# Kernel tuning notes

Measured on AMD Instinct MI355X. Metric: run time of the kernel, lower is better.

Reference implementation:

```python
import jax, jax.numpy as jnp
import numpy as np

D_MODEL = 1024
N_HEADS = 16
D_K = D_MODEL // N_HEADS
B, S = 8, 1024
EPS = 1e-8


def setup_inputs() -> dict:
    key = jax.random.key(0)
    ks = jax.random.split(key, 6)
    scale = 1.0 / np.sqrt(D_MODEL)
    return {
        "Q_in": jax.random.normal(ks[0], (B, S, D_MODEL), jnp.float32),
        "mask": jax.random.randint(ks[1], (B, 1, S, S), 0, 2, jnp.int32),
        "Wq": jax.random.normal(ks[2], (D_MODEL, D_MODEL), jnp.float32) * scale,
        "bq": jnp.zeros((D_MODEL,), jnp.float32),
        "Wk": jax.random.normal(ks[3], (D_MODEL, D_MODEL), jnp.float32) * scale,
        "bk": jnp.zeros((D_MODEL,), jnp.float32),
        "Wv": jax.random.normal(ks[4], (D_MODEL, D_MODEL), jnp.float32) * scale,
        "bv": jnp.zeros((D_MODEL,), jnp.float32),
        "Wo": jax.random.normal(ks[5], (D_MODEL, D_MODEL), jnp.float32) * scale,
        "bo": jnp.zeros((D_MODEL,), jnp.float32),
    }


def reference(Q_in, mask, Wq, bq, Wk, bk, Wv, bv, Wo, bo):
    # QKV projections: [B,S,D] -> [B,H,S,d_k]
    def split_heads(x):
        return x.reshape(B, S, N_HEADS, D_K).transpose(0, 2, 1, 3)

    Q = split_heads(Q_in @ Wq + bq)
    K = split_heads(Q_in @ Wk + bk)
    V = split_heads(Q_in @ Wv + bv)

    # scaled scores [B,H,S,S], standard softmax
    scores = jnp.einsum("bhqd,bhkd->bhqk", Q, K) / jnp.sqrt(
        jnp.asarray(D_K, jnp.float32))
    scores = jax.nn.softmax(scores, axis=-1)
    # non-standard: multiplicative mask AFTER softmax, then row renorm
    scores = scores * mask.astype(scores.dtype)
    attn = scores / (jnp.sum(scores, axis=-1, keepdims=True) + EPS)

    context = jnp.einsum("bhqk,bhkd->bhqd", attn, V)
    context = context.transpose(0, 2, 1, 3).reshape(B, S, D_MODEL)
    return context @ Wo + bo
```

## Files before the change

### kernel.cpp

```cpp
#include <hip/hip_runtime.h>
#include <hip/hip_bf16.h>
#include <stdint.h>

typedef __attribute__((ext_vector_type(4))) float f32x4;
typedef __attribute__((ext_vector_type(8))) __bf16 bf16x8;
typedef unsigned short u16;
typedef unsigned int u32;
typedef unsigned long long u64;

#define NH 16
#define DKK 64
#define QSCALE 0.18033688011112042f

__device__ __forceinline__ u16 f2bf(float f) {
    u32 u = __builtin_bit_cast(u32, f);
    u32 r = (u + 0x7fffu + ((u >> 16) & 1u)) >> 16;
    return (u16)r;
}

__device__ __forceinline__ u16 cvt_bf(float f) {
    __hip_bfloat16 h = __float2bfloat16(f);
    return *reinterpret_cast<u16*>(&h);
}

__device__ __forceinline__ float exp2_fast(float x) {
    return __builtin_amdgcn_exp2f(x);
}

__device__ __forceinline__ void gload16(const void* g, void* l) {
    __builtin_amdgcn_global_load_lds((const __attribute__((address_space(1))) void*)g,
                                     (__attribute__((address_space(3))) void*)l, 16, 0, 0);
}

__global__ __launch_bounds__(256) void k_prep(const float* __restrict__ x,
                                              u16* __restrict__ xb,
                                              const float* __restrict__ wq,
                                              const float* __restrict__ wk,
                                              const float* __restrict__ wv,
                                              const float* __restrict__ wo,
                                              u16* __restrict__ wt,
                                              const int* __restrict__ mask,
                                              u64* __restrict__ mb) {
    int bx = blockIdx.x;
    if (bx < 4096) {
        int i = bx * 256 + threadIdx.x;
        const float4* p = (const float4*)x + (size_t)i * 2;
        float4 a = p[0], b = p[1];
        union { u16 h[8]; uint4 q; } o;
        o.h[0] = f2bf(a.x); o.h[1] = f2bf(a.y); o.h[2] = f2bf(a.z); o.h[3] = f2bf(a.w);
        o.h[4] = f2bf(b.x); o.h[5] = f2bf(b.y); o.h[6] = f2bf(b.z); o.h[7] = f2bf(b.w);
        ((uint4*)xb)[i] = o.q;
    } else if (bx < 8192) {
        int idx = bx - 4096;
        int z = idx >> 10;
        const float* w = (z == 0) ? wq : (z == 1) ? wk : (z == 2) ? wv : wo;
        __shared__ float t[32][33];
        int tx = threadIdx.x & 31, ty = threadIdx.x >> 5;
        int n0 = (idx & 31) * 32, k0 = ((idx >> 5) & 31) * 32;
        for (int rr = 0; rr < 4; ++rr)
            t[ty + rr * 8][tx] = w[(size_t)(k0 + ty + rr * 8) * 1024 + n0 + tx];
        __syncthreads();
        for (int rr = 0; rr < 4; ++rr) {
            int n = n0 + ty + rr * 8;
            wt[((size_t)z * 1024 + n) * 1024 + k0 + tx] = f2bf(t[tx][ty + rr * 8]);
        }
    } else {
        int wid = ((bx - 8192) * 256 + threadIdx.x) >> 6;
        int lane = threadIdx.x & 63;
        for (int c = wid; c < 8 * 1024 * 16; c += 8192) {
            int m = mask[(size_t)c * 64 + lane];
            u64 bits = __ballot(m != 0);
            if (lane == 0)
                mb[(c & 0xFFFFC000u) | ((c & 15) << 10) | ((c >> 4) & 1023)] = bits;
        }
    }
}

template <int MODE>
__global__ __launch_bounds__(256) void k_gemm(const u16* __restrict__ A,
                                              const u16* __restrict__ Bt,
                                              const float* __restrict__ b0,
                                              const float* __restrict__ b1,
                                              const float* __restrict__ b2,
                                              u16* __restrict__ q_out,
                                              u16* __restrict__ k_out,
                                              u16* __restrict__ v_out,
                                              float* __restrict__ out) {
    __shared__ u16 As[128 * 32];
    __shared__ u16 Bs[128 * 32];
    int tid = threadIdx.x;
    int wv = tid >> 6, lane = tid & 63;
    int r = lane & 15, g = lane >> 4;
    int wr = wv >> 1, wc = wv & 1;
    int m0 = blockIdx.x * 128, n0 = blockIdx.y * 128;
    f32x4 acc[4][4] = {};
    for (int kt = 0; kt < 1024; kt += 32) {
        __syncthreads();
        for (int i = 0; i < 2; ++i) {
            int e = i * 256 + tid;
            int row = e >> 2;
            int cs = ((e & 3) ^ ((row >> 1) & 3)) * 8;
            const u16* ga = A + (size_t)(m0 + row) * 1024 + kt + cs;
            const u16* gb = Bt + (size_t)(n0 + row) * 1024 + kt + cs;
            gload16(ga, As + (size_t)(i * 256 + wv * 64) * 8);
            gload16(gb, Bs + (size_t)(i * 256 + wv * 64) * 8);
        }
        __syncthreads();
        bf16x8 aF[4], bF[4];
#pragma unroll
        for (int m = 0; m < 4; ++m) {
            int ro = wr * 64 + m * 16 + r;
            aF[m] = *(const bf16x8*)&As[ro * 32 + ((g ^ ((ro >> 1) & 3)) << 3)];
        }
#pragma unroll
        for (int n = 0; n < 4; ++n) {
            int ro = wc * 64 + n * 16 + r;
            bF[n] = *(const bf16x8*)&Bs[ro * 32 + ((g ^ ((ro >> 1) & 3)) << 3)];
        }
#pragma unroll
        for (int m = 0; m < 4; ++m)
#pragma unroll
            for (int n = 0; n < 4; ++n)
                acc[m][n] = __builtin_amdgcn_mfma_f32_16x16x32_bf16(aF[m], bF[n], acc[m][n], 0, 0, 0);
    }
    for (int m = 0; m < 4; ++m) {
        int rowb = m0 + wr * 64 + m * 16 + 4 * g;
        for (int n = 0; n < 4; ++n) {
            int col = n0 + wc * 64 + n * 16 + r;
            if (MODE == 0) {
                int w = col >> 10, cn = col & 1023;
                const float* bp = (w == 0) ? b0 : (w == 1) ? b1 : b2;
                u16* dst = (w == 0) ? q_out : (w == 1) ? k_out : v_out;
                float sc = (w == 0) ? QSCALE : 1.0f;
                int h = cn >> 6, d = cn & 63;
                float bias = bp[cn];
                for (int i = 0; i < 4; ++i) {
                    int row = rowb + i;
                    int b = row >> 10, s = row & 1023;
                    float v = (acc[m][n][i] + bias) * sc;
                    dst[((size_t)(b * NH + h) * 1024 + s) * 64 + d] = f2bf(v);
                }
            } else {
                float bias = b0[col];
                for (int i = 0; i < 4; ++i) {
                    int row = rowb + i;
                    out[(size_t)row * 1024 + col] = acc[m][n][i] + bias;
                }
            }
        }
    }
}

__global__ __launch_bounds__(256) void k_transpose_v(const u16* __restrict__ vb,
                                                     u16* __restrict__ vt) {
    __shared__ u16 t[64][72];
    int bh = blockIdx.y, s0 = blockIdx.x * 64;
    int tid = threadIdx.x;
    for (int i = 0; i < 2; ++i) {
        int e = i * 256 + tid;
        int row = e >> 3, ch = (e & 7) * 8;
        uint4 v = *(const uint4*)(vb + ((size_t)bh * 1024 + s0 + row) * 64 + ch);
        *(uint4*)&t[row][ch] = v;
    }
    __syncthreads();
    for (int i = 0; i < 2; ++i) {
        int e = i * 256 + tid;
        int d = e >> 3, ch = (e & 7) * 8;
        union { u16 h[8]; uint4 q; } o;
        for (int j = 0; j < 8; ++j) o.h[j] = t[ch + j][d];
        *(uint4*)(vt + ((size_t)bh * 64 + d) * 1024 + s0 + ch) = o.q;
    }
}

__global__ __launch_bounds__(256, 3) void k_attn(const u16* __restrict__ qb,
                                                 const u16* __restrict__ kb,
                                                 const u16* __restrict__ vt,
                                                 const u64* __restrict__ mbits,
                                                 u16* __restrict__ ctx) {
    __shared__ u16 Kd[2][64 * 64];
    __shared__ u16 Vd[2][64 * 64];
    int tid = threadIdx.x, wv = tid >> 6, lane = tid & 63;
    int r = lane & 15, g = lane >> 4;
    int q0 = blockIdx.x * 128, bh = blockIdx.y;
    int b = bh >> 4, h = bh & 15;

    bf16x8 aq[2][2];
#pragma unroll
    for (int qg = 0; qg < 2; ++qg) {
        const u16* qp = qb + ((size_t)bh * 1024 + q0 + wv * 32 + qg * 16 + r) * 64 + g * 8;
        aq[qg][0] = *(const bf16x8*)qp;
        aq[qg][1] = *(const bf16x8*)(qp + 32);
    }

    f32x4 of[2][4] = {};
    f32x4 zacc[2] = {};
    const bf16x8 vone = {(__bf16)1.f, (__bf16)1.f, (__bf16)1.f, (__bf16)1.f,
                         (__bf16)1.f, (__bf16)1.f, (__bf16)1.f, (__bf16)1.f};

    const u64* mrow = mbits + ((size_t)b * 16) * 1024 + q0 + wv * 32 + r;
    u64 mbc[2] = {mrow[0], mrow[16]};

    for (int i2 = 0; i2 < 2; ++i2) {
        int e = i2 * 256 + tid;
        int s = e >> 3, c = e & 7;
        int cs = (c ^ (s & 7)) * 8;
        int kr = (s & 0x20) | ((s & 0x0C) << 1) | ((s & 0x10) >> 2) | (s & 3);
        gload16(kb + ((size_t)bh * 1024 + kr) * 64 + cs, Kd[0] + (size_t)e * 8);
        gload16(vt + ((size_t)bh * 64 + s) * 1024 + cs, Vd[0] + (size_t)e * 8);
    }
    __syncthreads();

    for (int t = 0; t < 16; ++t) {
        int cur = t & 1;
        u64 mbn0 = 0, mbn1 = 0;
        if (t < 15) {
            int ktn = (t + 1) * 64;
            for (int i2 = 0; i2 < 2; ++i2) {
                int e = i2 * 256 + tid;
                int s = e >> 3, c = e & 7;
                int cs = (c ^ (s & 7)) * 8;
                int kr = (s & 0x20) | ((s & 0x0C) << 1) | ((s & 0x10) >> 2) | (s & 3);
                gload16(kb + ((size_t)bh * 1024 + ktn + kr) * 64 + cs, Kd[cur ^ 1] + (size_t)e * 8);
                gload16(vt + ((size_t)bh * 64 + s) * 1024 + ktn + cs, Vd[cur ^ 1] + (size_t)e * 8);
            }
            mbn0 = mrow[(size_t)(t + 1) * 1024];
            mbn1 = mrow[(size_t)(t + 1) * 1024 + 16];
        }
        const u16* K = Kd[cur];
        const u16* V = Vd[cur];

        bf16x8 bk0[4], bk1[4];
#pragma unroll
        for (int nf = 0; nf < 4; ++nf) {
            int rowk = (nf * 16 + r) * 64;
            bk0[nf] = *(const bf16x8*)&K[rowk + ((g ^ (r & 7)) << 3)];
            bk1[nf] = *(const bf16x8*)&K[rowk + (((g + 4) ^ (r & 7)) << 3)];
        }

        bf16x8 pfr[2][2];
#pragma unroll
        for (int qg = 0; qg < 2; ++qg) {
            f32x4 sf[4];
            __builtin_amdgcn_s_setprio(1);
#pragma unroll
            for (int nf = 0; nf < 4; ++nf) {
                f32x4 z = {0.f, 0.f, 0.f, 0.f};
                z = __builtin_amdgcn_mfma_f32_16x16x32_bf16(bk0[nf], aq[qg][0], z, 0, 0, 0);
                sf[nf] = __builtin_amdgcn_mfma_f32_16x16x32_bf16(bk1[nf], aq[qg][1], z, 0, 0, 0);
            }
            __builtin_amdgcn_s_setprio(0);
            u64 m64 = mbc[qg] >> (g * 8);
            u32 mlo = (u32)m64, mhi = (u32)(m64 >> 32);
            u32 pw[8];
#pragma unroll
            for (int nf = 0; nf < 4; ++nf) {
                u32 nib = ((nf & 2) ? mhi : mlo) >> ((nf & 1) * 4);
                u32 pm0 = ((nib & 1) ? 0xFFFFu : 0u) | ((nib & 2) ? 0xFFFF0000u : 0u);
                u32 pm1 = ((nib & 4) ? 0xFFFFu : 0u) | ((nib & 8) ? 0xFFFF0000u : 0u);
                float e0 = exp2_fast(sf[nf][0]), e1 = exp2_fast(sf[nf][1]);
                float e2 = exp2_fast(sf[nf][2]), e3 = exp2_fast(sf[nf][3]);
                pw[2 * nf]     = (((u32)cvt_bf(e0)) | ((u32)cvt_bf(e1) << 16)) & pm0;
                pw[2 * nf + 1] = (((u32)cvt_bf(e2)) | ((u32)cvt_bf(e3) << 16)) & pm1;
            }
            union { u32 w[4]; bf16x8 v; } f0, f1;
            f0.w[0] = pw[0]; f0.w[1] = pw[1]; f0.w[2] = pw[2]; f0.w[3] = pw[3];
            f1.w[0] = pw[4]; f1.w[1] = pw[5]; f1.w[2] = pw[6]; f1.w[3] = pw[7];
            pfr[qg][0] = f0.v;
            pfr[qg][1] = f1.v;
            __builtin_amdgcn_s_setprio(1);
            zacc[qg] = __builtin_amdgcn_mfma_f32_16x16x32_bf16(vone, pfr[qg][0], zacc[qg], 0, 0, 0);
            zacc[qg] = __builtin_amdgcn_mfma_f32_16x16x32_bf16(vone, pfr[qg][1], zacc[qg], 0, 0, 0);
            __builtin_amdgcn_s_setprio(0);
        }
        __builtin_amdgcn_s_setprio(1);
#pragma unroll
        for (int ks = 0; ks < 2; ++ks) {
#pragma unroll
            for (int nf = 0; nf < 4; ++nf) {
                bf16x8 av = *(const bf16x8*)&V[(nf * 16 + r) * 64 + (((ks * 4 + g) ^ (r & 7)) << 3)];
                of[0][nf] = __builtin_amdgcn_mfma_f32_16x16x32_bf16(av, pfr[0][ks], of[0][nf], 0, 0, 0);
                of[1][nf] = __builtin_amdgcn_mfma_f32_16x16x32_bf16(av, pfr[1][ks], of[1][nf], 0, 0, 0);
            }
        }
        __builtin_amdgcn_s_setprio(0);
        mbc[0] = mbn0;
        mbc[1] = mbn1;
        __syncthreads();
    }

#pragma unroll
    for (int qg = 0; qg < 2; ++qg) {
        float inv = 1.0f / zacc[qg][0];
        int qrow = q0 + wv * 32 + qg * 16 + r;
        u16* crow = ctx + ((size_t)(b * 1024 + qrow)) * 1024 + h * 64;
#pragma unroll
        for (int nf = 0; nf < 4; ++nf) {
            u32 w0 = ((u32)cvt_bf(of[qg][nf][0] * inv)) | ((u32)cvt_bf(of[qg][nf][1] * inv) << 16);
            u32 w1 = ((u32)cvt_bf(of[qg][nf][2] * inv)) | ((u32)cvt_bf(of[qg][nf][3] * inv) << 16);
            *(u32*)(crow + nf * 16 + g * 4) = w0;
            *(u32*)(crow + nf * 16 + g * 4 + 2) = w1;
        }
    }
}

extern "C" void kernel_launch(void* const* d_in, const int* in_sizes, int n_in,
                              void* d_out, int out_size, void* d_ws, size_t ws_size,
                              hipStream_t stream) {
    const float* Q_in = (const float*)d_in[0];
    const int*   mask = (const int*)d_in[1];
    const float* Wq = (const float*)d_in[2];
    const float* bq = (const float*)d_in[3];
    const float* Wk = (const float*)d_in[4];
    const float* bk = (const float*)d_in[5];
    const float* Wv = (const float*)d_in[6];
    const float* bv = (const float*)d_in[7];
    const float* Wo = (const float*)d_in[8];
    const float* bo = (const float*)d_in[9];

    char* ws = (char*)d_ws;
    u16* Xb = (u16*)(ws);
    u16* Wt = (u16*)(ws + 16777216);
    u16* Qb = (u16*)(ws + 25165824);
    u16* Kb = (u16*)(ws + 41943040);
    u16* Vb = (u16*)(ws + 58720256);
    u16* Vt = (u16*)(ws + 75497472);
    u64* Mb = (u64*)(ws + 92274688);
    u16* Ctx = Vb;

    k_prep<<<10240, 256, 0, stream>>>(Q_in, Xb, Wq, Wk, Wv, Wo, Wt, mask, Mb);
    k_gemm<0><<<dim3(64, 24), 256, 0, stream>>>(Xb, Wt, bq, bk, bv, Qb, Kb, Vb, nullptr);
    k_transpose_v<<<dim3(16, 128), 256, 0, stream>>>(Vb, Vt);
    k_attn<<<dim3(8, 128), 256, 0, stream>>>(Qb, Kb, Vt, Mb, Ctx);
    k_gemm<1><<<dim3(64, 8), 256, 0, stream>>>(Ctx, Wt + (size_t)3 * 1024 * 1024,
                                               bo, nullptr, nullptr,
                                               nullptr, nullptr, nullptr, (float*)d_out);
}
```

Measured before the change: 173.3 us.

## Triple-buffer GEMM LDS tiles with async global-to-LDS prefetch

Replaces the single-buffered K loop of the projection GEMM with a three-slot LDS ring. Loads for tile t+2 are issued before computing tile t, with vmcnt waits and a single barrier per iteration. Global load latency is meant to overlap with MFMA work instead of being exposed behind two barriers per step. Load addresses are also precomputed. The cost is three times the LDS for A and B (48KB), which may reduce occupancy, and the ordering relies on the waitcnt and barrier being correct.

```diff
diff --git a/kernel.cpp b/kernel.cpp
--- a/kernel.cpp
+++ b/kernel.cpp
@@ -86,43 +86,65 @@
                                               u16* __restrict__ k_out,
                                               u16* __restrict__ v_out,
                                               float* __restrict__ out) {
-    __shared__ u16 As[128 * 32];
-    __shared__ u16 Bs[128 * 32];
+    __shared__ u16 As[3][128 * 32];
+    __shared__ u16 Bs[3][128 * 32];
     int tid = threadIdx.x;
     int wv = tid >> 6, lane = tid & 63;
     int r = lane & 15, g = lane >> 4;
     int wr = wv >> 1, wc = wv & 1;
     int m0 = blockIdx.x * 128, n0 = blockIdx.y * 128;
     f32x4 acc[4][4] = {};
-    for (int kt = 0; kt < 1024; kt += 32) {
-        __syncthreads();
-        for (int i = 0; i < 2; ++i) {
-            int e = i * 256 + tid;
-            int row = e >> 2;
-            int cs = ((e & 3) ^ ((row >> 1) & 3)) * 8;
-            const u16* ga = A + (size_t)(m0 + row) * 1024 + kt + cs;
-            const u16* gb = Bt + (size_t)(n0 + row) * 1024 + kt + cs;
-            gload16(ga, As + (size_t)(i * 256 + wv * 64) * 8);
-            gload16(gb, Bs + (size_t)(i * 256 + wv * 64) * 8);
-        }
-        __syncthreads();
+
+    int row0 = tid >> 2, cs0 = (((tid & 3) ^ ((row0 >> 1) & 3))) * 8;
+    int row1 = (256 + tid) >> 2, cs1 = ((((256 + tid) & 3) ^ ((row1 >> 1) & 3))) * 8;
+    const u16* ga0 = A + (size_t)(m0 + row0) * 1024 + cs0;
+    const u16* ga1 = A + (size_t)(m0 + row1) * 1024 + cs1;
+    const u16* gb0 = Bt + (size_t)(n0 + row0) * 1024 + cs0;
+    const u16* gb1 = Bt + (size_t)(n0 + row1) * 1024 + cs1;
+
+#define GEMM_STAGE(slot, kt)                                   \
+    {                                                          \
+        gload16(ga0 + (kt), As[slot] + (size_t)tid * 8);       \
+        gload16(ga1 + (kt), As[slot] + (size_t)(256 + tid) * 8);\
+        gload16(gb0 + (kt), Bs[slot] + (size_t)tid * 8);       \
+        gload16(gb1 + (kt), Bs[slot] + (size_t)(256 + tid) * 8);\
+    }
+
+    GEMM_STAGE(0, 0);
+    GEMM_STAGE(1, 32);
+    asm volatile("s_waitcnt vmcnt(4)" ::: "memory");
+    __builtin_amdgcn_s_barrier();
+
+    int cur = 0, s2 = 2;
+    for (int t = 0; t < 32; ++t) {
+        if (t < 30) GEMM_STAGE(s2, (t + 2) * 32);
         bf16x8 aF[4], bF[4];
 #pragma unroll
         for (int m = 0; m < 4; ++m) {
             int ro = wr * 64 + m * 16 + r;
-            aF[m] = *(const bf16x8*)&As[ro * 32 + ((g ^ ((ro >> 1) & 3)) << 3)];
+            aF[m] = *(const bf16x8*)&As[cur][ro * 32 + ((g ^ ((ro >> 1) & 3)) << 3)];
         }
 #pragma unroll
         for (int n = 0; n < 4; ++n) {
             int ro = wc * 64 + n * 16 + r;
-            bF[n] = *(const bf16x8*)&Bs[ro * 32 + ((g ^ ((ro >> 1) & 3)) << 3)];
+            bF[n] = *(const bf16x8*)&Bs[cur][ro * 32 + ((g ^ ((ro >> 1) & 3)) << 3)];
         }
 #pragma unroll
         for (int m = 0; m < 4; ++m)
 #pragma unroll
             for (int n = 0; n < 4; ++n)
                 acc[m][n] = __builtin_amdgcn_mfma_f32_16x16x32_bf16(aF[m], bF[n], acc[m][n], 0, 0, 0);
-    }
+        if (t < 30) {
+            asm volatile("s_waitcnt vmcnt(4)" ::: "memory");
+        } else {
+            asm volatile("s_waitcnt vmcnt(0)" ::: "memory");
+        }
+        __builtin_amdgcn_s_barrier();
+        cur = (cur == 2) ? 0 : cur + 1;
+        s2 = (s2 == 2) ? 0 : s2 + 1;
+    }
+#undef GEMM_STAGE
+
     for (int m = 0; m < 4; ++m) {
         int rowb = m0 + wr * 64 + m * 16 + 4 * g;
         for (int n = 0; n < 4; ++n) {
```

After: 177.5 us. 1.02x slower.
